# Optimization experiments

Hardware: AMD Instinct MI355X
Metric: run time of the kernel (lower is better)

Reference implementation:

```python
import jax, jax.numpy as jnp
import numpy as np

N = 100000   # nodes (single node type 'word')
R = 4        # relation types (sorted rel_names)
E = 160000   # edges per relation
H = 128      # h_dim
O = 64       # out_dim


def setup_inputs() -> dict:
    key = jax.random.key(0)
    k0, k1, k2, k3 = jax.random.split(key, 4)
    embed = jax.random.normal(k0, (N, H), jnp.float32) * 0.1          # RelGraphEmbed table
    weight = jax.random.normal(k1, (R, H, O), jnp.float32) / np.sqrt(H)  # layer-2 per-rel weight
    bias1 = jnp.zeros((H,), jnp.float32)   # layer-1 h_bias
    bias2 = jnp.zeros((O,), jnp.float32)   # layer-2 h_bias
    edge_src = jax.random.randint(k2, (R, E), 0, N)
    edge_dst = jax.random.randint(k3, (R, E), 0, N)
    return dict(embed=embed, weight=weight, bias1=bias1, bias2=bias2,
                edge_src=edge_src, edge_dst=edge_dst)


def _rel_mean(x, src, dst, num_nodes):
    # GraphConv(norm='right'): sum messages into dst, divide by dst in-degree.
    msg = x[src]                                                    # [E, d] gather
    summed = jax.ops.segment_sum(msg, dst, num_segments=num_nodes)  # scatter-add
    deg = jax.ops.segment_sum(jnp.ones(src.shape, x.dtype), dst, num_segments=num_nodes)
    return summed / jnp.maximum(deg, 1.0)[:, None]


def reference(embed, weight, bias1, bias2, edge_src, edge_dst):
    n = embed.shape[0]
    # Layer 1: weight=False -> HeteroGraphConv sums right-normalized aggregations, then bias+relu.
    h1 = jnp.zeros_like(embed)
    for r in range(edge_src.shape[0]):
        h1 = h1 + _rel_mean(embed, edge_src[r], edge_dst[r], n)
    h1 = jax.nn.relu(h1 + bias1)
    # Layer 2: per-relation linear transform, aggregate, sum over relations, bias (no activation).
    out = jnp.zeros((n, weight.shape[-1]), embed.dtype)
    for r in range(edge_src.shape[0]):
        out = out + _rel_mean(h1 @ weight[r], edge_src[r], edge_dst[r], n)
    return out + bias2
```

## Files before the change

kernel.cpp:

```cpp
#include <hip/hip_runtime.h>
#include <hip/hip_bf16.h>

#define H 128
#define O 64
#define RELS 4

typedef short short8 __attribute__((ext_vector_type(8)));
typedef float f32x4 __attribute__((ext_vector_type(4)));
typedef unsigned int u32x4 __attribute__((ext_vector_type(4)));

static __device__ __forceinline__ unsigned short f2b(float x) {
    __hip_bfloat16 h = __float2bfloat16(x);
    return *reinterpret_cast<unsigned short*>(&h);
}
static __device__ __forceinline__ float blo(unsigned u) { return __uint_as_float(u << 16); }
static __device__ __forceinline__ float bhi(unsigned u) { return __uint_as_float(u & 0xffff0000u); }

#define ACC8(acc, uv, wt)                                           \
    acc[0] += (wt) * blo(uv.x); acc[1] += (wt) * bhi(uv.x);         \
    acc[2] += (wt) * blo(uv.y); acc[3] += (wt) * bhi(uv.y);         \
    acc[4] += (wt) * blo(uv.z); acc[5] += (wt) * bhi(uv.z);         \
    acc[6] += (wt) * blo(uv.w); acc[7] += (wt) * bhi(uv.w);

__global__ void k_prep(const float* __restrict__ embed, unsigned short* __restrict__ eb,
                       const float* __restrict__ W, unsigned short* __restrict__ WT,
                       const int* __restrict__ dst, int* __restrict__ cnt,
                       int n4, int wtot, int E, int RE, int N, int b_h, int b_cvt, int b_tot) {
    for (int b = blockIdx.x; b < b_tot; b += gridDim.x) {
        if (b < b_h) {
            int i = b * 256 + threadIdx.x;
            if (i < RE) { int r = i / E; atomicAdd(&cnt[r * N + dst[i]], 1); }
        } else if (b < b_h + b_cvt) {
            int base = (b - b_h) * 1024;
#pragma unroll
            for (int k = 0; k < 4; ++k) {
                int i = base + k * 256 + threadIdx.x;
                if (i < n4) {
                    f32x4 v = __builtin_nontemporal_load(((const f32x4*)embed) + i);
                    ushort4 o;
                    o.x = f2b(v[0]); o.y = f2b(v[1]); o.z = f2b(v[2]); o.w = f2b(v[3]);
                    ((ushort4*)eb)[i] = o;
                }
            }
        } else {
            int i = (b - b_h - b_cvt) * 256 + threadIdx.x;
            if (i < wtot) {
                int r = i >> 13;
                int n = (i >> 7) & (O - 1);
                int k = i & (H - 1);
                WT[i] = f2b(W[((size_t)r * H + k) * O + n]);
            }
        }
    }
}

__global__ void k_scan1(const int* __restrict__ cnt, int* __restrict__ offs,
                        int* __restrict__ bsum, int n, int N_) {
    __shared__ int sh[256];
    int t = threadIdx.x;
    int base = blockIdx.x * 1024 + t * 4;
    int4 v = make_int4(0, 0, 0, 0);
    if (base + 3 < n && (N_ & 3) == 0) {
#pragma unroll
        for (int r = 0; r < RELS; ++r) {
            int4 c = *(const int4*)(cnt + (size_t)r * N_ + base);
            v.x += c.x; v.y += c.y; v.z += c.z; v.w += c.w;
        }
    } else {
        for (int j = 0; j < 4; ++j) {
            int i = base + j;
            if (i < n) {
                int s = 0;
                for (int r = 0; r < RELS; ++r) s += cnt[(size_t)r * N_ + i];
                (&v.x)[j] = s;
            }
        }
    }
    int s = v.x + v.y + v.z + v.w;
    sh[t] = s; __syncthreads();
    for (int off = 1; off < 256; off <<= 1) {
        int x = (t >= off) ? sh[t - off] : 0;
        __syncthreads();
        sh[t] += x;
        __syncthreads();
    }
    int incl = sh[t];
    int ex = incl - s;
    if (base < n)     offs[base]     = ex;
    if (base + 1 < n) offs[base + 1] = ex + v.x;
    if (base + 2 < n) offs[base + 2] = ex + v.x + v.y;
    if (base + 3 < n) offs[base + 3] = ex + v.x + v.y + v.z;
    if (t == 255) bsum[blockIdx.x] = incl;
}

__global__ void k_scan2(int* __restrict__ bsum, int nb) {
    __shared__ int sh[512];
    int t = threadIdx.x;
    int s = (t < nb) ? bsum[t] : 0;
    sh[t] = s; __syncthreads();
    for (int off = 1; off < 512; off <<= 1) {
        int x = (t >= off) ? sh[t - off] : 0;
        __syncthreads();
        sh[t] += x;
        __syncthreads();
    }
    if (t < nb) bsum[t] = sh[t] - s;
}

__global__ void k_scan3c(int* __restrict__ offs, const int* __restrict__ bsum,
                         const int* __restrict__ cnt, int* __restrict__ cursor,
                         int n, int total, int N_) {
    int i = blockIdx.x * blockDim.x + threadIdx.x;
    if (i < n) {
        int off = offs[i] + bsum[i >> 10];
        offs[i] = off;
        int c0 = cnt[i], c1 = cnt[N_ + i], c2 = cnt[2 * N_ + i];
        cursor[i]          = off;
        cursor[N_ + i]     = off + c0;
        cursor[2 * N_ + i] = off + c0 + c1;
        cursor[3 * N_ + i] = off + c0 + c1 + c2;
    }
    if (i == 0) offs[n] = total;
}

__global__ void k_fill(const int* __restrict__ src, const int* __restrict__ dst,
                       const int* __restrict__ cnt, int* __restrict__ cursor,
                       uint2* __restrict__ ue, int E, int RE, int N) {
    for (int i = blockIdx.x * blockDim.x + threadIdx.x; i < RE; i += gridDim.x * blockDim.x) {
        int r = i / E;
        int d = dst[i];
        int pos = atomicAdd(&cursor[r * N + d], 1);
        float w = 1.0f / (float)max(cnt[r * N + d], 1);
        ue[pos] = make_uint2((unsigned)(r * N + src[i]), __float_as_uint(w));
    }
}

__global__ __launch_bounds__(256) void k_l1g(const unsigned short* __restrict__ eb,
                                             const int* __restrict__ offs2,
                                             const uint2* __restrict__ ue,
                                             const float* __restrict__ bias1,
                                             const unsigned short* __restrict__ WT,
                                             unsigned short* __restrict__ T,
                                             int N, int ntiles) {
    __shared__ __align__(16) unsigned short hs[2][16][136];
    __shared__ __align__(16) unsigned short st[4][16][72];
    int tid = threadIdx.x, wv = tid >> 6, l = tid & 63;
    int nloc = tid >> 4;
    int q = l & 15;
    int rA = l & 15, kb = (l >> 4) * 8;
    unsigned N1 = (unsigned)N, N2 = (unsigned)(2 * N);

    float4 b0 = *(const float4*)(bias1 + q * 8);
    float4 b1 = *(const float4*)(bias1 + q * 8 + 4);
    const unsigned short* Wb = WT + (size_t)wv * O * H;
    short8 bf[4][4];
#pragma unroll
    for (int nt = 0; nt < 4; ++nt)
#pragma unroll
        for (int kk = 0; kk < 4; ++kk)
            bf[nt][kk] = *(const short8*)(Wb + ((size_t)(nt * 16 + rA)) * H + kk * 32 + kb);

    int buf = 0;
    for (int tile = blockIdx.x; tile < ntiles; tile += gridDim.x, buf ^= 1) {
        int row0 = tile * 16;
        int node = row0 + nloc;

        float a[8] = {0.f, 0.f, 0.f, 0.f, 0.f, 0.f, 0.f, 0.f};
        float c[8] = {0.f, 0.f, 0.f, 0.f, 0.f, 0.f, 0.f, 0.f};
        if (node < N) {
            int2 be = *(const int2*)(offs2 + node);
            int beg = be.x, end = be.y;
            int e = beg;
            for (; e + 4 <= end; e += 4) {
                uint2 p0 = ue[e], p1 = ue[e + 1], p2 = ue[e + 2], p3 = ue[e + 3];
                unsigned s0 = p0.x; if (s0 >= N2) s0 -= N2; if (s0 >= N1) s0 -= N1;
                unsigned s1 = p1.x; if (s1 >= N2) s1 -= N2; if (s1 >= N1) s1 -= N1;
                unsigned s2 = p2.x; if (s2 >= N2) s2 -= N2; if (s2 >= N1) s2 -= N1;
                unsigned s3 = p3.x; if (s3 >= N2) s3 -= N2; if (s3 >= N1) s3 -= N1;
                float w0 = __uint_as_float(p0.y), w1 = __uint_as_float(p1.y);
                float w2 = __uint_as_float(p2.y), w3 = __uint_as_float(p3.y);
                uint4 u0 = *(const uint4*)(eb + (size_t)s0 * H + q * 8);
                uint4 u1 = *(const uint4*)(eb + (size_t)s1 * H + q * 8);
                uint4 u2 = *(const uint4*)(eb + (size_t)s2 * H + q * 8);
                uint4 u3 = *(const uint4*)(eb + (size_t)s3 * H + q * 8);
                ACC8(a, u0, w0);
                ACC8(c, u1, w1);
                ACC8(a, u2, w2);
                ACC8(c, u3, w3);
            }
            for (; e + 2 <= end; e += 2) {
                uint2 p0 = ue[e], p1 = ue[e + 1];
                unsigned s0 = p0.x; if (s0 >= N2) s0 -= N2; if (s0 >= N1) s0 -= N1;
                unsigned s1 = p1.x; if (s1 >= N2) s1 -= N2; if (s1 >= N1) s1 -= N1;
                float w0 = __uint_as_float(p0.y), w1 = __uint_as_float(p1.y);
                uint4 u0 = *(const uint4*)(eb + (size_t)s0 * H + q * 8);
                uint4 u1 = *(const uint4*)(eb + (size_t)s1 * H + q * 8);
                ACC8(a, u0, w0);
                ACC8(c, u1, w1);
            }
            if (e < end) {
                uint2 p0 = ue[e];
                unsigned s0 = p0.x; if (s0 >= N2) s0 -= N2; if (s0 >= N1) s0 -= N1;
                float w0 = __uint_as_float(p0.y);
                uint4 u0 = *(const uint4*)(eb + (size_t)s0 * H + q * 8);
                ACC8(a, u0, w0);
            }
            float f0 = fmaxf(a[0] + c[0] + b0.x, 0.f);
            float f1 = fmaxf(a[1] + c[1] + b0.y, 0.f);
            float f2 = fmaxf(a[2] + c[2] + b0.z, 0.f);
            float f3 = fmaxf(a[3] + c[3] + b0.w, 0.f);
            float f4 = fmaxf(a[4] + c[4] + b1.x, 0.f);
            float f5 = fmaxf(a[5] + c[5] + b1.y, 0.f);
            float f6 = fmaxf(a[6] + c[6] + b1.z, 0.f);
            float f7 = fmaxf(a[7] + c[7] + b1.w, 0.f);
            uint4 o;
            o.x = (unsigned)f2b(f0) | ((unsigned)f2b(f1) << 16);
            o.y = (unsigned)f2b(f2) | ((unsigned)f2b(f3) << 16);
            o.z = (unsigned)f2b(f4) | ((unsigned)f2b(f5) << 16);
            o.w = (unsigned)f2b(f6) | ((unsigned)f2b(f7) << 16);
            *(uint4*)&hs[buf][nloc][q * 8] = o;
        } else {
            uint4 zz = make_uint4(0, 0, 0, 0);
            *(uint4*)&hs[buf][nloc][q * 8] = zz;
        }
        __syncthreads();

        short8 af[4];
#pragma unroll
        for (int kk = 0; kk < 4; ++kk)
            af[kk] = *(const short8*)&hs[buf][rA][kk * 32 + kb];

        f32x4 z = {0.f, 0.f, 0.f, 0.f};
        f32x4 acc[4] = {z, z, z, z};
#pragma unroll
        for (int nt = 0; nt < 4; ++nt)
#pragma unroll
            for (int kk = 0; kk < 4; ++kk)
                acc[nt] = __builtin_amdgcn_mfma_f32_16x16x32_bf16(af[kk], bf[nt][kk], acc[nt], 0, 0, 0);

#pragma unroll
        for (int nt = 0; nt < 4; ++nt)
#pragma unroll
            for (int j = 0; j < 4; ++j)
                st[wv][(l >> 4) * 4 + j][nt * 16 + rA] = f2b(acc[nt][j]);

#pragma unroll
        for (int i = 0; i < 2; ++i) {
            int rr = i * 8 + (l >> 3);
            u32x4 v = *(const u32x4*)&st[wv][rr][(l & 7) * 8];
            int grow = row0 + rr;
            if (grow < N)
                __builtin_nontemporal_store(v, (u32x4*)(T + ((size_t)wv * N + grow) * O + (l & 7) * 8));
        }
    }
}

__global__ void k_pull2(const unsigned short* __restrict__ T, const int* __restrict__ offs2,
                        const uint2* __restrict__ ue, const float* __restrict__ bias2,
                        float* __restrict__ out, int N, int ngroups) {
    int o = threadIdx.x & 7;
    float4 b0 = *(const float4*)(bias2 + o * 8);
    float4 b1 = *(const float4*)(bias2 + o * 8 + 4);

    for (int g = blockIdx.x; g < ngroups; g += gridDim.x) {
        int node = g * 32 + (threadIdx.x >> 3);
        if (node >= N) continue;
        int2 be = *(const int2*)(offs2 + node);
        int beg = be.x, end = be.y;

        float a[8] = {0.f, 0.f, 0.f, 0.f, 0.f, 0.f, 0.f, 0.f};
        float c[8] = {0.f, 0.f, 0.f, 0.f, 0.f, 0.f, 0.f, 0.f};

        int e = beg;
        for (; e + 4 <= end; e += 4) {
            uint2 p0 = ue[e], p1 = ue[e + 1], p2 = ue[e + 2], p3 = ue[e + 3];
            float w0 = __uint_as_float(p0.y), w1 = __uint_as_float(p1.y);
            float w2 = __uint_as_float(p2.y), w3 = __uint_as_float(p3.y);
            uint4 u0 = *(const uint4*)(T + (size_t)p0.x * O + o * 8);
            uint4 u1 = *(const uint4*)(T + (size_t)p1.x * O + o * 8);
            uint4 u2 = *(const uint4*)(T + (size_t)p2.x * O + o * 8);
            uint4 u3 = *(const uint4*)(T + (size_t)p3.x * O + o * 8);
            ACC8(a, u0, w0);
            ACC8(c, u1, w1);
            ACC8(a, u2, w2);
            ACC8(c, u3, w3);
        }
        for (; e + 2 <= end; e += 2) {
            uint2 p0 = ue[e], p1 = ue[e + 1];
            float w0 = __uint_as_float(p0.y), w1 = __uint_as_float(p1.y);
            uint4 u0 = *(const uint4*)(T + (size_t)p0.x * O + o * 8);
            uint4 u1 = *(const uint4*)(T + (size_t)p1.x * O + o * 8);
            ACC8(a, u0, w0);
            ACC8(c, u1, w1);
        }
        if (e < end) {
            uint2 p0 = ue[e];
            float w0 = __uint_as_float(p0.y);
            uint4 u0 = *(const uint4*)(T + (size_t)p0.x * O + o * 8);
            ACC8(a, u0, w0);
        }

        f32x4 v0, v1;
        v0[0] = a[0] + c[0] + b0.x; v0[1] = a[1] + c[1] + b0.y;
        v0[2] = a[2] + c[2] + b0.z; v0[3] = a[3] + c[3] + b0.w;
        v1[0] = a[4] + c[4] + b1.x; v1[1] = a[5] + c[5] + b1.y;
        v1[2] = a[6] + c[6] + b1.z; v1[3] = a[7] + c[7] + b1.w;
        __builtin_nontemporal_store(v0, (f32x4*)(out + (size_t)node * O + o * 8));
        __builtin_nontemporal_store(v1, (f32x4*)(out + (size_t)node * O + o * 8 + 4));
    }
}

extern "C" void kernel_launch(void* const* d_in, const int* in_sizes, int n_in,
                              void* d_out, int out_size, void* d_ws, size_t ws_size,
                              hipStream_t stream) {
    const float* embed  = (const float*)d_in[0];
    const float* weight = (const float*)d_in[1];
    const float* bias1  = (const float*)d_in[2];
    const float* bias2  = (const float*)d_in[3];
    const int*   esrc   = (const int*)d_in[4];
    const int*   edst   = (const int*)d_in[5];
    float* out = (float*)d_out;

    const int N = in_sizes[0] / H;
    const int E = in_sizes[4] / RELS;
    const int RN = RELS * N;
    const int RE = RELS * E;

    char* p = (char*)d_ws;
    auto alloc = [&](size_t bytes) {
        char* q = p;
        p += (bytes + 255) & ~(size_t)255;
        return q;
    };
    int* cnt    = (int*)alloc((size_t)RN * 4);
    int* offs2  = (int*)alloc(((size_t)N + 1) * 4);
    int* cursor = (int*)alloc((size_t)RN * 4);
    int* bsum   = (int*)alloc(4096);
    uint2* ue   = (uint2*)alloc((size_t)RE * 8);
    unsigned short* eb  = (unsigned short*)alloc((size_t)N * H * 2);
    unsigned short* WT  = (unsigned short*)alloc((size_t)RELS * O * H * 2);
    unsigned short* T   = (unsigned short*)alloc((size_t)RELS * N * O * 2);

    hipMemsetAsync(cnt, 0, (size_t)RN * 4, stream);

    int n4 = N * H / 4;
    int wtot = RELS * O * H;
    int b_h   = (RE + 255) / 256;
    int b_cvt = (n4 + 1023) / 1024;
    int b_w   = (wtot + 255) / 256;
    int b_tot = b_h + b_cvt + b_w;
    int gprep = b_tot < 2048 ? b_tot : 2048;
    k_prep<<<gprep, 256, 0, stream>>>(embed, eb, weight, WT, edst, cnt,
                                      n4, wtot, E, RE, N, b_h, b_cvt, b_tot);

    int nb = (N + 1023) / 1024;
    k_scan1<<<nb, 256, 0, stream>>>(cnt, offs2, bsum, N, N);
    k_scan2<<<1, 512, 0, stream>>>(bsum, nb);
    k_scan3c<<<(N + 255) / 256, 256, 0, stream>>>(offs2, bsum, cnt, cursor, N, RE, N);

    int bfill = (RE + 255) / 256;
    k_fill<<<(bfill < 2048 ? bfill : 2048), 256, 0, stream>>>(esrc, edst, cnt, cursor, ue, E, RE, N);

    int ntiles = (N + 15) / 16;
    k_l1g<<<(ntiles < 2048 ? ntiles : 2048), 256, 0, stream>>>(eb, offs2, ue, bias1, WT, T, N, ntiles);

    int ngroups = (N + 31) / 32;
    k_pull2<<<(ngroups < 2048 ? ngroups : 2048), 256, 0, stream>>>(T, offs2, ue, bias2, out, N, ngroups);
}
```

Baseline: 170.5 us.

## Fuse block-sum scan into scan3c, dynamic tile scheduling in l1g, flat pull2 grid

Each block of scan3c now scans the per-block sums redundantly in shared memory, which folds k_scan2 into it and removes a launch. k_l1g swaps its static grid-stride tile loop for an atomic work counter, prefetching the next tile index into double-buffered shared memory to balance uneven in-degree. It also reloads the weight fragments from global/L1 per tile instead of holding them in registers, which lowers register pressure but adds loads. k_pull2 launches one block per 32-node group instead of a grid-stride loop.

```diff
diff --git a/kernel.cpp b/kernel.cpp
--- a/kernel.cpp
+++ b/kernel.cpp
@@ -93,26 +93,27 @@
     if (t == 255) bsum[blockIdx.x] = incl;
 }
 
-__global__ void k_scan2(int* __restrict__ bsum, int nb) {
-    __shared__ int sh[512];
+__global__ void k_scan3c(int* __restrict__ offs, const int* __restrict__ bsum, int nb,
+                         const int* __restrict__ cnt, int* __restrict__ cursor,
+                         int* __restrict__ ctr, int n, int total, int N_) {
+    __shared__ int sb[256];
     int t = threadIdx.x;
     int s = (t < nb) ? bsum[t] : 0;
-    sh[t] = s; __syncthreads();
-    for (int off = 1; off < 512; off <<= 1) {
-        int x = (t >= off) ? sh[t - off] : 0;
-        __syncthreads();
-        sh[t] += x;
-        __syncthreads();
-    }
-    if (t < nb) bsum[t] = sh[t] - s;
-}
-
-__global__ void k_scan3c(int* __restrict__ offs, const int* __restrict__ bsum,
-                         const int* __restrict__ cnt, int* __restrict__ cursor,
-                         int n, int total, int N_) {
-    int i = blockIdx.x * blockDim.x + threadIdx.x;
+    sb[t] = s; __syncthreads();
+    for (int off = 1; off < 256; off <<= 1) {
+        int x = (t >= off) ? sb[t - off] : 0;
+        __syncthreads();
+        sb[t] += x;
+        __syncthreads();
+    }
+    int ex = sb[t] - s;
+    __syncthreads();
+    sb[t] = ex;
+    __syncthreads();
+
+    int i = blockIdx.x * blockDim.x + t;
     if (i < n) {
-        int off = offs[i] + bsum[i >> 10];
+        int off = offs[i] + sb[i >> 10];
         offs[i] = off;
         int c0 = cnt[i], c1 = cnt[N_ + i], c2 = cnt[2 * N_ + i];
         cursor[i]          = off;
@@ -120,7 +121,7 @@
         cursor[2 * N_ + i] = off + c0 + c1;
         cursor[3 * N_ + i] = off + c0 + c1 + c2;
     }
-    if (i == 0) offs[n] = total;
+    if (i == 0) { offs[n] = total; ctr[0] = 0; }
 }
 
 __global__ void k_fill(const int* __restrict__ src, const int* __restrict__ dst,
@@ -141,9 +142,11 @@
                                              const float* __restrict__ bias1,
                                              const unsigned short* __restrict__ WT,
                                              unsigned short* __restrict__ T,
+                                             int* __restrict__ ctr,
                                              int N, int ntiles) {
     __shared__ __align__(16) unsigned short hs[2][16][136];
     __shared__ __align__(16) unsigned short st[4][16][72];
+    __shared__ int s_tile[2];
     int tid = threadIdx.x, wv = tid >> 6, l = tid & 63;
     int nloc = tid >> 4;
     int q = l & 15;
@@ -153,15 +156,16 @@
     float4 b0 = *(const float4*)(bias1 + q * 8);
     float4 b1 = *(const float4*)(bias1 + q * 8 + 4);
     const unsigned short* Wb = WT + (size_t)wv * O * H;
-    short8 bf[4][4];
-#pragma unroll
-    for (int nt = 0; nt < 4; ++nt)
-#pragma unroll
-        for (int kk = 0; kk < 4; ++kk)
-            bf[nt][kk] = *(const short8*)(Wb + ((size_t)(nt * 16 + rA)) * H + kk * 32 + kb);
-
-    int buf = 0;
-    for (int tile = blockIdx.x; tile < ntiles; tile += gridDim.x, buf ^= 1) {
+
+    if (tid == 0) s_tile[0] = atomicAdd(ctr, 1);
+    __syncthreads();
+
+    int p = 0;
+    for (;;) {
+        int tile = s_tile[p];
+        if (tile >= ntiles) break;
+        if (tid == 0) s_tile[p ^ 1] = atomicAdd(ctr, 1);
+
         int row0 = tile * 16;
         int node = row0 + nloc;
 
@@ -218,25 +222,30 @@
             o.y = (unsigned)f2b(f2) | ((unsigned)f2b(f3) << 16);
             o.z = (unsigned)f2b(f4) | ((unsigned)f2b(f5) << 16);
             o.w = (unsigned)f2b(f6) | ((unsigned)f2b(f7) << 16);
-            *(uint4*)&hs[buf][nloc][q * 8] = o;
+            *(uint4*)&hs[p][nloc][q * 8] = o;
         } else {
             uint4 zz = make_uint4(0, 0, 0, 0);
-            *(uint4*)&hs[buf][nloc][q * 8] = zz;
+            *(uint4*)&hs[p][nloc][q * 8] = zz;
         }
         __syncthreads();
 
         short8 af[4];
 #pragma unroll
         for (int kk = 0; kk < 4; ++kk)
-            af[kk] = *(const short8*)&hs[buf][rA][kk * 32 + kb];
+            af[kk] = *(const short8*)&hs[p][rA][kk * 32 + kb];
 
         f32x4 z = {0.f, 0.f, 0.f, 0.f};
         f32x4 acc[4] = {z, z, z, z};
 #pragma unroll
-        for (int nt = 0; nt < 4; ++nt)
+        for (int nt = 0; nt < 4; ++nt) {
+            short8 bfr[4];
 #pragma unroll
             for (int kk = 0; kk < 4; ++kk)
-                acc[nt] = __builtin_amdgcn_mfma_f32_16x16x32_bf16(af[kk], bf[nt][kk], acc[nt], 0, 0, 0);
+                bfr[kk] = *(const short8*)(Wb + ((size_t)(nt * 16 + rA)) * H + kk * 32 + kb);
+#pragma unroll
+            for (int kk = 0; kk < 4; ++kk)
+                acc[nt] = __builtin_amdgcn_mfma_f32_16x16x32_bf16(af[kk], bfr[kk], acc[nt], 0, 0, 0);
+        }
 
 #pragma unroll
         for (int nt = 0; nt < 4; ++nt)
@@ -252,62 +261,60 @@
             if (grow < N)
                 __builtin_nontemporal_store(v, (u32x4*)(T + ((size_t)wv * N + grow) * O + (l & 7) * 8));
         }
+        p ^= 1;
     }
 }
 
 __global__ void k_pull2(const unsigned short* __restrict__ T, const int* __restrict__ offs2,
                         const uint2* __restrict__ ue, const float* __restrict__ bias2,
-                        float* __restrict__ out, int N, int ngroups) {
+                        float* __restrict__ out, int N) {
+    int node = blockIdx.x * 32 + (threadIdx.x >> 3);
+    if (node >= N) return;
     int o = threadIdx.x & 7;
+    int2 be = *(const int2*)(offs2 + node);
+    int beg = be.x, end = be.y;
+
+    float a[8] = {0.f, 0.f, 0.f, 0.f, 0.f, 0.f, 0.f, 0.f};
+    float c[8] = {0.f, 0.f, 0.f, 0.f, 0.f, 0.f, 0.f, 0.f};
+
+    int e = beg;
+    for (; e + 4 <= end; e += 4) {
+        uint2 p0 = ue[e], p1 = ue[e + 1], p2 = ue[e + 2], p3 = ue[e + 3];
+        float w0 = __uint_as_float(p0.y), w1 = __uint_as_float(p1.y);
+        float w2 = __uint_as_float(p2.y), w3 = __uint_as_float(p3.y);
+        uint4 u0 = *(const uint4*)(T + (size_t)p0.x * O + o * 8);
+        uint4 u1 = *(const uint4*)(T + (size_t)p1.x * O + o * 8);
+        uint4 u2 = *(const uint4*)(T + (size_t)p2.x * O + o * 8);
+        uint4 u3 = *(const uint4*)(T + (size_t)p3.x * O + o * 8);
+        ACC8(a, u0, w0);
+        ACC8(c, u1, w1);
+        ACC8(a, u2, w2);
+        ACC8(c, u3, w3);
+    }
+    for (; e + 2 <= end; e += 2) {
+        uint2 p0 = ue[e], p1 = ue[e + 1];
+        float w0 = __uint_as_float(p0.y), w1 = __uint_as_float(p1.y);
+        uint4 u0 = *(const uint4*)(T + (size_t)p0.x * O + o * 8);
+        uint4 u1 = *(const uint4*)(T + (size_t)p1.x * O + o * 8);
+        ACC8(a, u0, w0);
+        ACC8(c, u1, w1);
+    }
+    if (e < end) {
+        uint2 p0 = ue[e];
+        float w0 = __uint_as_float(p0.y);
+        uint4 u0 = *(const uint4*)(T + (size_t)p0.x * O + o * 8);
+        ACC8(a, u0, w0);
+    }
+
     float4 b0 = *(const float4*)(bias2 + o * 8);
     float4 b1 = *(const float4*)(bias2 + o * 8 + 4);
-
-    for (int g = blockIdx.x; g < ngroups; g += gridDim.x) {
-        int node = g * 32 + (threadIdx.x >> 3);
-        if (node >= N) continue;
-        int2 be = *(const int2*)(offs2 + node);
-        int beg = be.x, end = be.y;
-
-        float a[8] = {0.f, 0.f, 0.f, 0.f, 0.f, 0.f, 0.f, 0.f};
-        float c[8] = {0.f, 0.f, 0.f, 0.f, 0.f, 0.f, 0.f, 0.f};
-
-        int e = beg;
-        for (; e + 4 <= end; e += 4) {
-            uint2 p0 = ue[e], p1 = ue[e + 1], p2 = ue[e + 2], p3 = ue[e + 3];
-            float w0 = __uint_as_float(p0.y), w1 = __uint_as_float(p1.y);
-            float w2 = __uint_as_float(p2.y), w3 = __uint_as_float(p3.y);
-            uint4 u0 = *(const uint4*)(T + (size_t)p0.x * O + o * 8);
-            uint4 u1 = *(const uint4*)(T + (size_t)p1.x * O + o * 8);
-            uint4 u2 = *(const uint4*)(T + (size_t)p2.x * O + o * 8);
-            uint4 u3 = *(const uint4*)(T + (size_t)p3.x * O + o * 8);
-            ACC8(a, u0, w0);
-            ACC8(c, u1, w1);
-            ACC8(a, u2, w2);
-            ACC8(c, u3, w3);
-        }
-        for (; e + 2 <= end; e += 2) {
-            uint2 p0 = ue[e], p1 = ue[e + 1];
-            float w0 = __uint_as_float(p0.y), w1 = __uint_as_float(p1.y);
-            uint4 u0 = *(const uint4*)(T + (size_t)p0.x * O + o * 8);
-            uint4 u1 = *(const uint4*)(T + (size_t)p1.x * O + o * 8);
-            ACC8(a, u0, w0);
-            ACC8(c, u1, w1);
-        }
-        if (e < end) {
-            uint2 p0 = ue[e];
-            float w0 = __uint_as_float(p0.y);
-            uint4 u0 = *(const uint4*)(T + (size_t)p0.x * O + o * 8);
-            ACC8(a, u0, w0);
-        }
-
-        f32x4 v0, v1;
-        v0[0] = a[0] + c[0] + b0.x; v0[1] = a[1] + c[1] + b0.y;
-        v0[2] = a[2] + c[2] + b0.z; v0[3] = a[3] + c[3] + b0.w;
-        v1[0] = a[4] + c[4] + b1.x; v1[1] = a[5] + c[5] + b1.y;
-        v1[2] = a[6] + c[6] + b1.z; v1[3] = a[7] + c[7] + b1.w;
-        __builtin_nontemporal_store(v0, (f32x4*)(out + (size_t)node * O + o * 8));
-        __builtin_nontemporal_store(v1, (f32x4*)(out + (size_t)node * O + o * 8 + 4));
-    }
+    f32x4 v0, v1;
+    v0[0] = a[0] + c[0] + b0.x; v0[1] = a[1] + c[1] + b0.y;
+    v0[2] = a[2] + c[2] + b0.z; v0[3] = a[3] + c[3] + b0.w;
+    v1[0] = a[4] + c[4] + b1.x; v1[1] = a[5] + c[5] + b1.y;
+    v1[2] = a[6] + c[6] + b1.z; v1[3] = a[7] + c[7] + b1.w;
+    __builtin_nontemporal_store(v0, (f32x4*)(out + (size_t)node * O + o * 8));
+    __builtin_nontemporal_store(v1, (f32x4*)(out + (size_t)node * O + o * 8 + 4));
 }
 
 extern "C" void kernel_launch(void* const* d_in, const int* in_sizes, int n_in,
@@ -336,6 +343,7 @@
     int* offs2  = (int*)alloc(((size_t)N + 1) * 4);
     int* cursor = (int*)alloc((size_t)RN * 4);
     int* bsum   = (int*)alloc(4096);
+    int* ctr    = (int*)alloc(256);
     uint2* ue   = (uint2*)alloc((size_t)RE * 8);
     unsigned short* eb  = (unsigned short*)alloc((size_t)N * H * 2);
     unsigned short* WT  = (unsigned short*)alloc((size_t)RELS * O * H * 2);
@@ -355,15 +363,14 @@
 
     int nb = (N + 1023) / 1024;
     k_scan1<<<nb, 256, 0, stream>>>(cnt, offs2, bsum, N, N);
-    k_scan2<<<1, 512, 0, stream>>>(bsum, nb);
-    k_scan3c<<<(N + 255) / 256, 256, 0, stream>>>(offs2, bsum, cnt, cursor, N, RE, N);
+    k_scan3c<<<(N + 255) / 256, 256, 0, stream>>>(offs2, bsum, nb, cnt, cursor, ctr, N, RE, N);
 
     int bfill = (RE + 255) / 256;
     k_fill<<<(bfill < 2048 ? bfill : 2048), 256, 0, stream>>>(esrc, edst, cnt, cursor, ue, E, RE, N);
 
     int ntiles = (N + 15) / 16;
-    k_l1g<<<(ntiles < 2048 ? ntiles : 2048), 256, 0, stream>>>(eb, offs2, ue, bias1, WT, T, N, ntiles);
+    k_l1g<<<(ntiles < 2048 ? ntiles : 2048), 256, 0, stream>>>(eb, offs2, ue, bias1, WT, T, ctr, N, ntiles);
 
     int ngroups = (N + 31) / 32;
-    k_pull2<<<(ngroups < 2048 ? ngroups : 2048), 256, 0, stream>>>(T, offs2, ue, bias2, out, N, ngroups);
-}
+    k_pull2<<<ngroups, 256, 0, stream>>>(T, offs2, ue, bias2, out, N);
+}
```

Result: slower. 210.7 us (+23.6%).
